# Kernel tuning notes

Measured on AMD Instinct MI355X. Metric: run time of the kernel, lower is better.

The kernel has to match this reference:

```python
import jax, jax.numpy as jnp
import numpy as np

H = 512          # hidden_size
SF = 4           # scale_factor
B, S, L = 16, 2048, 2

def setup_inputs() -> dict:
    key = jax.random.key(0)
    ks = jax.random.split(key, 9)
    return {
        "hidden": jax.random.normal(ks[0], (L, B, H * SF), dtype=jnp.float32),
        "encoder_outputs": jax.random.normal(ks[1], (B, S, H * SF), dtype=jnp.float32),
        "We": jax.random.normal(ks[2], (H, H * SF), dtype=jnp.float32) * 0.02,
        "be": jax.random.normal(ks[3], (H,), dtype=jnp.float32) * 0.02,
        "Wh": jax.random.normal(ks[4], (H, H * SF), dtype=jnp.float32) * 0.02,
        "bh": jax.random.normal(ks[5], (H,), dtype=jnp.float32) * 0.02,
        "Wa": jax.random.normal(ks[6], (H, 2 * H), dtype=jnp.float32) * 0.02,
        "ba": jax.random.normal(ks[7], (H,), dtype=jnp.float32) * 0.02,
        "v": jax.random.uniform(ks[8], (1, H), dtype=jnp.float32),
    }

def reference(hidden, encoder_outputs, We, be, Wh, bh, Wa, ba, v):
    # hidden[-1]: [B, 4H] -> [B, H]
    h = hidden[-1] @ Wh.T + bh
    # encoder_outputs: [B, S, 4H] -> [B, S, H]
    eo = jnp.einsum('bsf,hf->bsh', encoder_outputs, We) + be
    # concat([h broadcast to S, eo]) @ Wa.T == h @ Wa_h.T + eo @ Wa_e.T (split concat matmul)
    Wa_h, Wa_e = Wa[:, :H], Wa[:, H:]
    energy = jnp.tanh(h[:, None, :] @ Wa_h.T + jnp.einsum('bsh,kh->bsk', eo, Wa_e) + ba)  # [B,S,H]
    scores = jnp.einsum('bsh,h->bs', energy, v[0])           # [B,S]
    attn_weights = jax.nn.softmax(scores, axis=1)            # [B,S]
    context_vector = jnp.einsum('bs,bsh->bh', attn_weights, eo)  # [B,H]
    return (context_vector, attn_weights)
```

## Files before the change

### kernel.cpp

```cpp
#include <hip/hip_runtime.h>

#define HH 512
#define FF 2048
#define BB 16
#define SS 2048
#define MM 32768

using f32x4 = __attribute__((ext_vector_type(4))) float;
using s16x8 = __attribute__((ext_vector_type(8))) short;

struct __align__(8)  US4 { unsigned short x, y, z, w; };
struct __align__(16) US8 { unsigned short s[8]; };

__device__ __forceinline__ unsigned short f2bf(float f) {
  unsigned int u = __builtin_bit_cast(unsigned int, f);
  u += 0x7fffu + ((u >> 16) & 1u);
  return (unsigned short)(u >> 16);
}
__device__ __forceinline__ float bf2f(unsigned short u) {
  unsigned int x = ((unsigned int)u) << 16;
  return __builtin_bit_cast(float, x);
}
__device__ __forceinline__ void gload_lds16(const void* g, void* l) {
  __builtin_amdgcn_global_load_lds(
      (const __attribute__((address_space(1))) unsigned int*)g,
      (__attribute__((address_space(3))) unsigned int*)l, 16, 0, 0);
}

__global__ void k_conv_we(const float* __restrict__ W, unsigned short* __restrict__ O) {
  int idx = blockIdx.x * 256 + threadIdx.x;
  f32x4 x = *(const f32x4*)(W + idx * 4);
  US4 p{f2bf(x.x), f2bf(x.y), f2bf(x.z), f2bf(x.w)};
  *(US4*)(O + idx * 4) = p;
}
__global__ void k_conv_wae(const float* __restrict__ Wa, unsigned short* __restrict__ O) {
  int idx = blockIdx.x * 256 + threadIdx.x;
  int k = idx >> 7, h4 = idx & 127;
  f32x4 x = *(const f32x4*)(Wa + k * 1024 + 512 + h4 * 4);
  US4 p{f2bf(x.x), f2bf(x.y), f2bf(x.z), f2bf(x.w)};
  *(US4*)(O + idx * 4) = p;
}

__global__ void k_h(const float* __restrict__ hidden, const float* __restrict__ Wh,
                    const float* __restrict__ bh, float* __restrict__ h_ws) {
  int t = threadIdx.x, lane = t & 63, wid = t >> 6;
  int out = blockIdx.x * 4 + wid;
  int b = out >> 9, j = out & 511;
  const float* hr = hidden + (1) * BB * FF + b * FF;
  const float* wr = Wh + j * FF;
  float a = 0.f;
#pragma unroll
  for (int i = 0; i < 8; ++i) {
    int o = i * 256 + lane * 4;
    f32x4 x = *(const f32x4*)(hr + o);
    f32x4 y = *(const f32x4*)(wr + o);
    a += x.x * y.x + x.y * y.y + x.z * y.z + x.w * y.w;
  }
#pragma unroll
  for (int m = 32; m; m >>= 1) a += __shfl_xor(a, m);
  if (lane == 0) h_ws[out] = a + bh[j];
}

__global__ void k_bb(const float* __restrict__ h_ws, const float* __restrict__ Wa,
                     const float* __restrict__ ba, float* __restrict__ bb_ws) {
  int t = threadIdx.x, lane = t & 63, wid = t >> 6;
  int out = blockIdx.x * 4 + wid;
  int b = out >> 9, k = out & 511;
  const float* hr = h_ws + b * HH;
  const float* wa = Wa + k * 1024;
  float a = 0.f;
#pragma unroll
  for (int i = 0; i < 2; ++i) {
    int o = i * 256 + lane * 4;
    f32x4 x = *(const f32x4*)(hr + o);
    f32x4 y = *(const f32x4*)(wa + o);
    a += x.x * y.x + x.y * y.y + x.z * y.z + x.w * y.w;
  }
#pragma unroll
  for (int m = 32; m; m >>= 1) a += __shfl_xor(a, m);
  if (lane == 0) bb_ws[out] = a + ba[k];
}

__global__ __launch_bounds__(512, 4) void k_gemm1(
    const float* __restrict__ enc, const unsigned short* __restrict__ Web,
    const float* __restrict__ be, unsigned short* __restrict__ eo) {
  __shared__ unsigned short smem[36864];
  unsigned short* As = smem;
  unsigned short* Bs = smem + 4096;
  const int t = threadIdx.x, lane = t & 63, wid = t >> 6;
  const int m0 = blockIdx.x * 64;
  f32x4 acc[4][4] = {};

  f32x4 areg[2];
#pragma unroll
  for (int i = 0; i < 2; ++i) {
    int idx = i * 512 + t, row = idx >> 4, c4 = idx & 15;
    areg[i] = *(const f32x4*)(enc + (size_t)(m0 + row) * FF + c4 * 4);
  }

#pragma unroll 1
  for (int kt = 0; kt < FF; kt += 64) {
#pragma unroll
    for (int i = 0; i < 8; ++i) {
      int idx = i * 512 + t, row = idx >> 3, c = idx & 7;
      int sc = c ^ (row & 7);
      gload_lds16(Web + (size_t)row * FF + kt + sc * 8, Bs + idx * 8);
    }
#pragma unroll
    for (int i = 0; i < 2; ++i) {
      int idx = i * 512 + t, row = idx >> 4, c4 = idx & 15;
      f32x4 x = areg[i];
      US4 p{f2bf(x.x), f2bf(x.y), f2bf(x.z), f2bf(x.w)};
      int byte = row * 128 + ((c4 * 8) ^ ((row & 7) << 4));
      *(US4*)((char*)As + byte) = p;
    }
    {
      int ktn = (kt + 64 < FF) ? kt + 64 : 0;
#pragma unroll
      for (int i = 0; i < 2; ++i) {
        int idx = i * 512 + t, row = idx >> 4, c4 = idx & 15;
        areg[i] = *(const f32x4*)(enc + (size_t)(m0 + row) * FF + ktn + c4 * 4);
      }
    }
    __syncthreads();
#pragma unroll
    for (int ks = 0; ks < 2; ++ks) {
      s16x8 af[4], bfr[4];
#pragma unroll
      for (int mi = 0; mi < 4; ++mi) {
        int row = mi * 16 + (lane & 15);
        int byte = row * 128 + ((ks * 64 + (lane >> 4) * 16) ^ ((row & 7) << 4));
        af[mi] = *(const s16x8*)((const char*)As + byte);
      }
#pragma unroll
      for (int ni = 0; ni < 4; ++ni) {
        int row = wid * 64 + ni * 16 + (lane & 15);
        int byte = row * 128 + ((ks * 64 + (lane >> 4) * 16) ^ ((row & 7) << 4));
        bfr[ni] = *(const s16x8*)((const char*)Bs + byte);
      }
#pragma unroll
      for (int mi = 0; mi < 4; ++mi)
#pragma unroll
        for (int ni = 0; ni < 4; ++ni)
          acc[mi][ni] = __builtin_amdgcn_mfma_f32_16x16x32_bf16(af[mi], bfr[ni], acc[mi][ni], 0, 0, 0);
    }
    __syncthreads();
  }

  unsigned short* Cs = smem;
#pragma unroll
  for (int ni = 0; ni < 4; ++ni) {
    int col = wid * 64 + ni * 16 + (lane & 15);
    float bev = be[col];
#pragma unroll
    for (int mi = 0; mi < 4; ++mi)
#pragma unroll
      for (int j = 0; j < 4; ++j) {
        int row = mi * 16 + (lane >> 4) * 4 + j;
        Cs[row * 512 + col] = f2bf(acc[mi][ni][j] + bev);
      }
  }
  __syncthreads();
#pragma unroll
  for (int i = 0; i < 8; ++i) {
    int idx = i * 512 + t, row = idx >> 6, c = idx & 63;
    *(US8*)(eo + (size_t)(m0 + row) * HH + c * 8) = *(const US8*)(Cs + row * 512 + c * 8);
  }
}

__global__ __launch_bounds__(256, 2) void k_gemm2(
    const unsigned short* __restrict__ eo, const unsigned short* __restrict__ Waeb,
    const float* __restrict__ bbw, const float* __restrict__ vv,
    float* __restrict__ sp) {
  __shared__ unsigned short smem[128 * 64 * 2];
  __shared__ float part[2][128];
  unsigned short* As = smem;
  unsigned short* Bs = smem + 128 * 64;
  const int t = threadIdx.x, lane = t & 63;
  const int wid = t >> 6, wr = wid >> 1, wc = wid & 1;
  const int bid = blockIdx.x;
  const int n0 = (bid & 3) * 128;
  const int m0 = (bid >> 2) * 128;
  const int b = m0 >> 11;
  f32x4 acc[4][4] = {};

#pragma unroll 1
  for (int kt = 0; kt < HH; kt += 64) {
#pragma unroll
    for (int i = 0; i < 4; ++i) {
      int idx = i * 256 + t, row = idx >> 3, c = idx & 7;
      int sc = c ^ (row & 7);
      gload_lds16(eo + (size_t)(m0 + row) * HH + kt + sc * 8, As + idx * 8);
    }
#pragma unroll
    for (int i = 0; i < 4; ++i) {
      int idx = i * 256 + t, row = idx >> 3, c = idx & 7;
      int sc = c ^ (row & 7);
      gload_lds16(Waeb + (size_t)(n0 + row) * HH + kt + sc * 8, Bs + idx * 8);
    }
    __syncthreads();
#pragma unroll
    for (int ks = 0; ks < 2; ++ks) {
      s16x8 af[4], bfr[4];
#pragma unroll
      for (int mi = 0; mi < 4; ++mi) {
        int row = wr * 64 + mi * 16 + (lane & 15);
        int byte = row * 128 + ((ks * 64 + (lane >> 4) * 16) ^ ((row & 7) << 4));
        af[mi] = *(const s16x8*)((const char*)As + byte);
      }
#pragma unroll
      for (int ni = 0; ni < 4; ++ni) {
        int row = wc * 64 + ni * 16 + (lane & 15);
        int byte = row * 128 + ((ks * 64 + (lane >> 4) * 16) ^ ((row & 7) << 4));
        bfr[ni] = *(const s16x8*)((const char*)Bs + byte);
      }
#pragma unroll
      for (int mi = 0; mi < 4; ++mi)
#pragma unroll
        for (int ni = 0; ni < 4; ++ni)
          acc[mi][ni] = __builtin_amdgcn_mfma_f32_16x16x32_bf16(af[mi], bfr[ni], acc[mi][ni], 0, 0, 0);
    }
    __syncthreads();
  }

  float vcol[4], bcol[4];
#pragma unroll
  for (int ni = 0; ni < 4; ++ni) {
    int col = n0 + wc * 64 + ni * 16 + (lane & 15);
    vcol[ni] = vv[col];
    bcol[ni] = bbw[b * HH + col];
  }
  float ps[4][4];
#pragma unroll
  for (int mi = 0; mi < 4; ++mi)
#pragma unroll
    for (int j = 0; j < 4; ++j) {
      float s = 0.f;
#pragma unroll
      for (int ni = 0; ni < 4; ++ni)
        s += tanhf(acc[mi][ni][j] + bcol[ni]) * vcol[ni];
      ps[mi][j] = s;
    }
#pragma unroll
  for (int m = 1; m < 16; m <<= 1)
#pragma unroll
    for (int mi = 0; mi < 4; ++mi)
#pragma unroll
      for (int j = 0; j < 4; ++j) ps[mi][j] += __shfl_xor(ps[mi][j], m);
  if ((lane & 15) == 0) {
#pragma unroll
    for (int mi = 0; mi < 4; ++mi)
#pragma unroll
      for (int j = 0; j < 4; ++j)
        part[wc][wr * 64 + mi * 16 + (lane >> 4) * 4 + j] = ps[mi][j];
  }
  __syncthreads();
  if (t < 128) sp[(bid & 3) * MM + m0 + t] = part[0][t] + part[1][t];
}

__global__ void k_softmax(const float* __restrict__ sp, float* __restrict__ attn) {
  const int b = blockIdx.x, t = threadIdx.x, lane = t & 63, wid = t >> 6;
  __shared__ float red[4];
  float vals[8], lmax = -3.0e38f;
#pragma unroll
  for (int i = 0; i < 8; ++i) {
    int s = t + i * 256;
    float x = sp[b * SS + s] + sp[MM + b * SS + s] + sp[2 * MM + b * SS + s] + sp[3 * MM + b * SS + s];
    vals[i] = x;
    lmax = fmaxf(lmax, x);
  }
#pragma unroll
  for (int m = 32; m; m >>= 1) lmax = fmaxf(lmax, __shfl_xor(lmax, m));
  if (lane == 0) red[wid] = lmax;
  __syncthreads();
  lmax = fmaxf(fmaxf(red[0], red[1]), fmaxf(red[2], red[3]));
  __syncthreads();
  float lsum = 0.f;
#pragma unroll
  for (int i = 0; i < 8; ++i) {
    vals[i] = __expf(vals[i] - lmax);
    lsum += vals[i];
  }
#pragma unroll
  for (int m = 32; m; m >>= 1) lsum += __shfl_xor(lsum, m);
  if (lane == 0) red[wid] = lsum;
  __syncthreads();
  float inv = 1.0f / (red[0] + red[1] + red[2] + red[3]);
#pragma unroll
  for (int i = 0; i < 8; ++i) attn[b * SS + t + i * 256] = vals[i] * inv;
}

__global__ __launch_bounds__(512) void k_ctx1(const unsigned short* __restrict__ eo,
                                              const float* __restrict__ attn,
                                              float* __restrict__ cp) {
  __shared__ float red[8][512];
  const int b = blockIdx.x >> 3, ch = blockIdx.x & 7, t = threadIdx.x;
  const int tg = t & 63, sg = t >> 6;
  const float* aw = attn + b * SS + ch * 256;
  float acc[8] = {};
  for (int s = sg; s < 256; s += 8) {
    float w = aw[s];
    US8 vv = *(const US8*)(eo + (size_t)(b * SS + ch * 256 + s) * HH + tg * 8);
#pragma unroll
    for (int j = 0; j < 8; ++j) acc[j] += w * bf2f(vv.s[j]);
  }
#pragma unroll
  for (int j = 0; j < 8; ++j) red[sg][tg * 8 + j] = acc[j];
  __syncthreads();
  float a = 0.f;
#pragma unroll
  for (int g = 0; g < 8; ++g) a += red[g][t];
  cp[blockIdx.x * HH + t] = a;
}

__global__ void k_ctx2(const float* __restrict__ cp, float* __restrict__ ctx) {
  const int b = blockIdx.x, h = threadIdx.x;
  float a = 0.f;
#pragma unroll
  for (int c = 0; c < 8; ++c) a += cp[(b * 8 + c) * HH + h];
  ctx[b * HH + h] = a;
}

extern "C" void kernel_launch(void* const* d_in, const int* in_sizes, int n_in,
                              void* d_out, int out_size, void* d_ws, size_t ws_size,
                              hipStream_t stream) {
  (void)in_sizes; (void)n_in; (void)out_size; (void)ws_size;
  const float* hidden = (const float*)d_in[0];
  const float* enc    = (const float*)d_in[1];
  const float* We     = (const float*)d_in[2];
  const float* be     = (const float*)d_in[3];
  const float* Wh     = (const float*)d_in[4];
  const float* bh     = (const float*)d_in[5];
  const float* Wa     = (const float*)d_in[6];
  const float* ba     = (const float*)d_in[7];
  const float* v      = (const float*)d_in[8];

  float* out  = (float*)d_out;
  float* ctx  = out;
  float* attn = out + BB * HH;

  char* ws = (char*)d_ws;
  unsigned short* Web  = (unsigned short*)ws;  ws += (size_t)HH * FF * 2;
  unsigned short* Waeb = (unsigned short*)ws;  ws += (size_t)HH * HH * 2;
  float* h_ws  = (float*)ws;                   ws += (size_t)BB * HH * 4;
  float* bb_ws = (float*)ws;                   ws += (size_t)BB * HH * 4;
  unsigned short* eo = (unsigned short*)ws;    ws += (size_t)MM * HH * 2;
  float* sp = (float*)ws;                      ws += (size_t)4 * MM * 4;
  float* cp = (float*)ws;                      ws += (size_t)BB * 8 * HH * 4;

  k_conv_we<<<1024, 256, 0, stream>>>(We, Web);
  k_conv_wae<<<256, 256, 0, stream>>>(Wa, Waeb);
  k_h<<<2048, 256, 0, stream>>>(hidden, Wh, bh, h_ws);
  k_bb<<<2048, 256, 0, stream>>>(h_ws, Wa, ba, bb_ws);
  k_gemm1<<<512, 512, 0, stream>>>(enc, Web, be, eo);
  k_gemm2<<<1024, 256, 0, stream>>>(eo, Waeb, bb_ws, v, sp);
  k_softmax<<<16, 256, 0, stream>>>(sp, attn);
  k_ctx1<<<128, 512, 0, stream>>>(eo, attn, cp);
  k_ctx2<<<16, 512, 0, stream>>>(cp, ctx);
}
```

Before: 179.1 us.

## Fuse energy GEMM into encoder GEMM with double-buffered pipelined main loop

Merges the second GEMM (eo·Wa_e, tanh, v-dot) into the first GEMM's epilogue. The eo tile stays in LDS and full-width score rows are produced per block, which removes the eo re-read and the four-way partial-score buffer. The main K-loop is rewritten with double-buffered LDS, async global-to-LDS loads and explicit waitcnt/barrier scheduling to overlap loads with MFMA. Weight conversions are merged into one launch and the context reduction gets finer chunking. In exchange, LDS use is larger and occupancy lower, and the second-GEMM B operand is read directly from global memory.

New measurement: 187.3 us. 4.6% more time.

```diff
diff --git a/kernel.cpp b/kernel.cpp
--- a/kernel.cpp
+++ b/kernel.cpp
@@ -1,4 +1,5 @@
 #include <hip/hip_runtime.h>
+#include <math.h>
 
 #define HH 512
 #define FF 2048
@@ -27,18 +28,21 @@
       (__attribute__((address_space(3))) unsigned int*)l, 16, 0, 0);
 }
 
-__global__ void k_conv_we(const float* __restrict__ W, unsigned short* __restrict__ O) {
-  int idx = blockIdx.x * 256 + threadIdx.x;
-  f32x4 x = *(const f32x4*)(W + idx * 4);
-  US4 p{f2bf(x.x), f2bf(x.y), f2bf(x.z), f2bf(x.w)};
-  *(US4*)(O + idx * 4) = p;
-}
-__global__ void k_conv_wae(const float* __restrict__ Wa, unsigned short* __restrict__ O) {
-  int idx = blockIdx.x * 256 + threadIdx.x;
-  int k = idx >> 7, h4 = idx & 127;
-  f32x4 x = *(const f32x4*)(Wa + k * 1024 + 512 + h4 * 4);
-  US4 p{f2bf(x.x), f2bf(x.y), f2bf(x.z), f2bf(x.w)};
-  *(US4*)(O + idx * 4) = p;
+__global__ void k_conv(const float* __restrict__ We, const float* __restrict__ Wa,
+                       unsigned short* __restrict__ OWe, unsigned short* __restrict__ OWa) {
+  int bid = blockIdx.x, t = threadIdx.x;
+  if (bid < 1024) {
+    int idx = bid * 256 + t;
+    f32x4 x = *(const f32x4*)(We + (size_t)idx * 4);
+    US4 p{f2bf(x.x), f2bf(x.y), f2bf(x.z), f2bf(x.w)};
+    *(US4*)(OWe + (size_t)idx * 4) = p;
+  } else {
+    int idx = (bid - 1024) * 256 + t;
+    int k = idx >> 7, h4 = idx & 127;
+    f32x4 x = *(const f32x4*)(Wa + (size_t)k * 1024 + 512 + h4 * 4);
+    US4 p{f2bf(x.x), f2bf(x.y), f2bf(x.z), f2bf(x.w)};
+    *(US4*)(OWa + (size_t)idx * 4) = p;
+  }
 }
 
 __global__ void k_h(const float* __restrict__ hidden, const float* __restrict__ Wh,
@@ -47,7 +51,7 @@
   int out = blockIdx.x * 4 + wid;
   int b = out >> 9, j = out & 511;
   const float* hr = hidden + (1) * BB * FF + b * FF;
-  const float* wr = Wh + j * FF;
+  const float* wr = Wh + (size_t)j * FF;
   float a = 0.f;
 #pragma unroll
   for (int i = 0; i < 8; ++i) {
@@ -67,7 +71,7 @@
   int out = blockIdx.x * 4 + wid;
   int b = out >> 9, k = out & 511;
   const float* hr = h_ws + b * HH;
-  const float* wa = Wa + k * 1024;
+  const float* wa = Wa + (size_t)k * 1024;
   float a = 0.f;
 #pragma unroll
   for (int i = 0; i < 2; ++i) {
@@ -81,73 +85,125 @@
   if (lane == 0) bb_ws[out] = a + ba[k];
 }
 
-__global__ __launch_bounds__(512, 4) void k_gemm1(
+
+template<int CUR, bool IB, bool IA, int WN>
+__device__ __forceinline__ void gstep(const float* enc_m0, const unsigned short* Web,
+                                      unsigned short* smem, int kt, int t, int lane, int wid,
+                                      f32x4* regC, f32x4* regN, f32x4 (&acc)[4][4]) {
+  unsigned short* Asc = smem + (CUR ? 4096 : 0);
+  unsigned short* Asn = smem + (CUR ? 0 : 4096);
+  unsigned short* Bsc = smem + (CUR ? 40960 : 8192);
+  unsigned short* Bsn = smem + (CUR ? 8192 : 40960);
+  asm volatile("s_waitcnt vmcnt(%0)" :: "i"(WN) : "memory");
+  __builtin_amdgcn_sched_barrier(0);
+  __builtin_amdgcn_s_barrier();
+  if (IB) {
+#pragma unroll
+    for (int i = 0; i < 8; ++i) {
+      int idx = i * 512 + t, row = idx >> 3, c = idx & 7, sc = c ^ (row & 7);
+      gload_lds16(Web + (size_t)row * FF + (kt + 64) + sc * 8, Bsn + idx * 8);
+    }
+  }
+  __builtin_amdgcn_sched_barrier(0);
+  if (IA) {
+#pragma unroll
+    for (int i = 0; i < 2; ++i) {
+      int idx = i * 512 + t, row = idx >> 4, c4 = idx & 15;
+      regN[i] = *(const f32x4*)(enc_m0 + (size_t)row * FF + (kt + 128) + c4 * 4);
+    }
+  }
+  __builtin_amdgcn_sched_barrier(0);
+#pragma unroll
+  for (int ks = 0; ks < 2; ++ks) {
+    s16x8 af[4], bfr[4];
+#pragma unroll
+    for (int mi = 0; mi < 4; ++mi) {
+      int row = mi * 16 + (lane & 15);
+      int byte = row * 128 + (((ks * 64) + (lane >> 4) * 16) ^ ((row & 7) << 4));
+      af[mi] = *(const s16x8*)((const char*)Asc + byte);
+    }
+#pragma unroll
+    for (int ni = 0; ni < 4; ++ni) {
+      int row = wid * 64 + ni * 16 + (lane & 15);
+      int byte = row * 128 + (((ks * 64) + (lane >> 4) * 16) ^ ((row & 7) << 4));
+      bfr[ni] = *(const s16x8*)((const char*)Bsc + byte);
+    }
+#pragma unroll
+    for (int mi = 0; mi < 4; ++mi)
+#pragma unroll
+      for (int ni = 0; ni < 4; ++ni)
+        acc[mi][ni] = __builtin_amdgcn_mfma_f32_16x16x32_bf16(af[mi], bfr[ni], acc[mi][ni], 0, 0, 0);
+  }
+  if (IB) {
+#pragma unroll
+    for (int i = 0; i < 2; ++i) {
+      int idx = i * 512 + t, row = idx >> 4, c4 = idx & 15;
+      f32x4 x = regC[i];
+      US4 p{f2bf(x.x), f2bf(x.y), f2bf(x.z), f2bf(x.w)};
+      int byte = row * 128 + ((c4 * 8) ^ ((row & 7) << 4));
+      *(US4*)((char*)Asn + byte) = p;
+    }
+  }
+  asm volatile("s_waitcnt lgkmcnt(0)" ::: "memory");
+  __builtin_amdgcn_sched_barrier(0);
+  __builtin_amdgcn_s_barrier();
+}
+
+__global__ __launch_bounds__(512, 2) void k_gemm1f(
     const float* __restrict__ enc, const unsigned short* __restrict__ Web,
-    const float* __restrict__ be, unsigned short* __restrict__ eo) {
-  __shared__ unsigned short smem[36864];
-  unsigned short* As = smem;
-  unsigned short* Bs = smem + 4096;
+    const float* __restrict__ be, const unsigned short* __restrict__ Waeb,
+    const float* __restrict__ bbw, const float* __restrict__ vv,
+    unsigned short* __restrict__ eo, float* __restrict__ sp) {
+  __shared__ unsigned short smem[73728];
   const int t = threadIdx.x, lane = t & 63, wid = t >> 6;
   const int m0 = blockIdx.x * 64;
+  const float* enc_m0 = enc + (size_t)m0 * FF;
+  unsigned short* As0 = smem;
+  unsigned short* Bs0 = smem + 8192;
   f32x4 acc[4][4] = {};
-
-  f32x4 areg[2];
+  f32x4 areg0[2], areg1[2], aP[2];
+
 #pragma unroll
   for (int i = 0; i < 2; ++i) {
     int idx = i * 512 + t, row = idx >> 4, c4 = idx & 15;
-    areg[i] = *(const f32x4*)(enc + (size_t)(m0 + row) * FF + c4 * 4);
-  }
-
+    aP[i] = *(const f32x4*)(enc_m0 + (size_t)row * FF + c4 * 4);
+  }
+  __builtin_amdgcn_sched_barrier(0);
+#pragma unroll
+  for (int i = 0; i < 8; ++i) {
+    int idx = i * 512 + t, row = idx >> 3, c = idx & 7, sc = c ^ (row & 7);
+    gload_lds16(Web + (size_t)row * FF + sc * 8, Bs0 + idx * 8);
+  }
+  __builtin_amdgcn_sched_barrier(0);
+#pragma unroll
+  for (int i = 0; i < 2; ++i) {
+    int idx = i * 512 + t, row = idx >> 4, c4 = idx & 15;
+    areg1[i] = *(const f32x4*)(enc_m0 + (size_t)row * FF + 64 + c4 * 4);
+  }
+  __builtin_amdgcn_sched_barrier(0);
+#pragma unroll
+  for (int i = 0; i < 2; ++i) {
+    int idx = i * 512 + t, row = idx >> 4, c4 = idx & 15;
+    f32x4 x = aP[i];
+    US4 p{f2bf(x.x), f2bf(x.y), f2bf(x.z), f2bf(x.w)};
+    int byte = row * 128 + ((c4 * 8) ^ ((row & 7) << 4));
+    *(US4*)((char*)As0 + byte) = p;
+  }
+  asm volatile("s_waitcnt lgkmcnt(0)" ::: "memory");
+  __builtin_amdgcn_sched_barrier(0);
+  __builtin_amdgcn_s_barrier();
+
+  int kt = 0;
 #pragma unroll 1
-  for (int kt = 0; kt < FF; kt += 64) {
-#pragma unroll
-    for (int i = 0; i < 8; ++i) {
-      int idx = i * 512 + t, row = idx >> 3, c = idx & 7;
-      int sc = c ^ (row & 7);
-      gload_lds16(Web + (size_t)row * FF + kt + sc * 8, Bs + idx * 8);
-    }
-#pragma unroll
-    for (int i = 0; i < 2; ++i) {
-      int idx = i * 512 + t, row = idx >> 4, c4 = idx & 15;
-      f32x4 x = areg[i];
-      US4 p{f2bf(x.x), f2bf(x.y), f2bf(x.z), f2bf(x.w)};
-      int byte = row * 128 + ((c4 * 8) ^ ((row & 7) << 4));
-      *(US4*)((char*)As + byte) = p;
-    }
-    {
-      int ktn = (kt + 64 < FF) ? kt + 64 : 0;
-#pragma unroll
-      for (int i = 0; i < 2; ++i) {
-        int idx = i * 512 + t, row = idx >> 4, c4 = idx & 15;
-        areg[i] = *(const f32x4*)(enc + (size_t)(m0 + row) * FF + ktn + c4 * 4);
-      }
-    }
-    __syncthreads();
-#pragma unroll
-    for (int ks = 0; ks < 2; ++ks) {
-      s16x8 af[4], bfr[4];
-#pragma unroll
-      for (int mi = 0; mi < 4; ++mi) {
-        int row = mi * 16 + (lane & 15);
-        int byte = row * 128 + ((ks * 64 + (lane >> 4) * 16) ^ ((row & 7) << 4));
-        af[mi] = *(const s16x8*)((const char*)As + byte);
-      }
-#pragma unroll
-      for (int ni = 0; ni < 4; ++ni) {
-        int row = wid * 64 + ni * 16 + (lane & 15);
-        int byte = row * 128 + ((ks * 64 + (lane >> 4) * 16) ^ ((row & 7) << 4));
-        bfr[ni] = *(const s16x8*)((const char*)Bs + byte);
-      }
-#pragma unroll
-      for (int mi = 0; mi < 4; ++mi)
-#pragma unroll
-        for (int ni = 0; ni < 4; ++ni)
-          acc[mi][ni] = __builtin_amdgcn_mfma_f32_16x16x32_bf16(af[mi], bfr[ni], acc[mi][ni], 0, 0, 0);
-    }
-    __syncthreads();
-  }
-
-  unsigned short* Cs = smem;
+  for (int tt = 0; tt < 15; ++tt) {
+    gstep<0, true, true, 2>(enc_m0, Web, smem, kt, t, lane, wid, areg1, areg0, acc);
+    gstep<1, true, true, 2>(enc_m0, Web, smem, kt + 64, t, lane, wid, areg0, areg1, acc);
+    kt += 128;
+  }
+  gstep<0, true, false, 2>(enc_m0, Web, smem, 1920, t, lane, wid, areg1, areg0, acc);
+  gstep<1, false, false, 0>(enc_m0, Web, smem, 1984, t, lane, wid, areg0, areg1, acc);
+
+  unsigned short* Cs = smem + 40960;
 #pragma unroll
   for (int ni = 0; ni < 4; ++ni) {
     int col = wid * 64 + ni * 16 + (lane & 15);
@@ -157,76 +213,50 @@
 #pragma unroll
       for (int j = 0; j < 4; ++j) {
         int row = mi * 16 + (lane >> 4) * 4 + j;
-        Cs[row * 512 + col] = f2bf(acc[mi][ni][j] + bev);
+        int byte = row * 1024 + ((col * 2) ^ ((row & 7) << 4));
+        *(unsigned short*)((char*)Cs + byte) = f2bf(acc[mi][ni][j] + bev);
       }
   }
   __syncthreads();
+
 #pragma unroll
   for (int i = 0; i < 8; ++i) {
     int idx = i * 512 + t, row = idx >> 6, c = idx & 63;
-    *(US8*)(eo + (size_t)(m0 + row) * HH + c * 8) = *(const US8*)(Cs + row * 512 + c * 8);
-  }
-}
-
-__global__ __launch_bounds__(256, 2) void k_gemm2(
-    const unsigned short* __restrict__ eo, const unsigned short* __restrict__ Waeb,
-    const float* __restrict__ bbw, const float* __restrict__ vv,
-    float* __restrict__ sp) {
-  __shared__ unsigned short smem[128 * 64 * 2];
-  __shared__ float part[2][128];
-  unsigned short* As = smem;
-  unsigned short* Bs = smem + 128 * 64;
-  const int t = threadIdx.x, lane = t & 63;
-  const int wid = t >> 6, wr = wid >> 1, wc = wid & 1;
-  const int bid = blockIdx.x;
-  const int n0 = (bid & 3) * 128;
-  const int m0 = (bid >> 2) * 128;
+    int byte = row * 1024 + ((c * 16) ^ ((row & 7) << 4));
+    *(US8*)(eo + (size_t)(m0 + row) * HH + c * 8) = *(const US8*)((const char*)Cs + byte);
+  }
+
+  f32x4 acc2[4][4] = {};
+#pragma unroll 1
+  for (int kt2 = 0; kt2 < HH; kt2 += 64) {
+#pragma unroll
+    for (int ks = 0; ks < 2; ++ks) {
+      int k2 = kt2 + ks * 32 + (lane >> 4) * 8;
+      s16x8 af[4], bfr[4];
+#pragma unroll
+      for (int mi = 0; mi < 4; ++mi) {
+        int row = mi * 16 + (lane & 15);
+        int byte = row * 1024 + ((k2 * 2) ^ ((row & 7) << 4));
+        af[mi] = *(const s16x8*)((const char*)Cs + byte);
+      }
+#pragma unroll
+      for (int ni = 0; ni < 4; ++ni) {
+        int nrow = wid * 64 + ni * 16 + (lane & 15);
+        bfr[ni] = *(const s16x8*)(Waeb + (size_t)nrow * HH + k2);
+      }
+#pragma unroll
+      for (int mi = 0; mi < 4; ++mi)
+#pragma unroll
+        for (int ni = 0; ni < 4; ++ni)
+          acc2[mi][ni] = __builtin_amdgcn_mfma_f32_16x16x32_bf16(af[mi], bfr[ni], acc2[mi][ni], 0, 0, 0);
+    }
+  }
+
   const int b = m0 >> 11;
-  f32x4 acc[4][4] = {};
-
-#pragma unroll 1
-  for (int kt = 0; kt < HH; kt += 64) {
-#pragma unroll
-    for (int i = 0; i < 4; ++i) {
-      int idx = i * 256 + t, row = idx >> 3, c = idx & 7;
-      int sc = c ^ (row & 7);
-      gload_lds16(eo + (size_t)(m0 + row) * HH + kt + sc * 8, As + idx * 8);
-    }
-#pragma unroll
-    for (int i = 0; i < 4; ++i) {
-      int idx = i * 256 + t, row = idx >> 3, c = idx & 7;
-      int sc = c ^ (row & 7);
-      gload_lds16(Waeb + (size_t)(n0 + row) * HH + kt + sc * 8, Bs + idx * 8);
-    }
-    __syncthreads();
-#pragma unroll
-    for (int ks = 0; ks < 2; ++ks) {
-      s16x8 af[4], bfr[4];
-#pragma unroll
-      for (int mi = 0; mi < 4; ++mi) {
-        int row = wr * 64 + mi * 16 + (lane & 15);
-        int byte = row * 128 + ((ks * 64 + (lane >> 4) * 16) ^ ((row & 7) << 4));
-        af[mi] = *(const s16x8*)((const char*)As + byte);
-      }
-#pragma unroll
-      for (int ni = 0; ni < 4; ++ni) {
-        int row = wc * 64 + ni * 16 + (lane & 15);
-        int byte = row * 128 + ((ks * 64 + (lane >> 4) * 16) ^ ((row & 7) << 4));
-        bfr[ni] = *(const s16x8*)((const char*)Bs + byte);
-      }
-#pragma unroll
-      for (int mi = 0; mi < 4; ++mi)
-#pragma unroll
-        for (int ni = 0; ni < 4; ++ni)
-          acc[mi][ni] = __builtin_amdgcn_mfma_f32_16x16x32_bf16(af[mi], bfr[ni], acc[mi][ni], 0, 0, 0);
-    }
-    __syncthreads();
-  }
-
   float vcol[4], bcol[4];
 #pragma unroll
   for (int ni = 0; ni < 4; ++ni) {
-    int col = n0 + wc * 64 + ni * 16 + (lane & 15);
+    int col = wid * 64 + ni * 16 + (lane & 15);
     vcol[ni] = vv[col];
     bcol[ni] = bbw[b * HH + col];
   }
@@ -238,7 +268,7 @@
       float s = 0.f;
 #pragma unroll
       for (int ni = 0; ni < 4; ++ni)
-        s += tanhf(acc[mi][ni][j] + bcol[ni]) * vcol[ni];
+        s += tanhf(acc2[mi][ni][j] + bcol[ni]) * vcol[ni];
       ps[mi][j] = s;
     }
 #pragma unroll
@@ -247,15 +277,21 @@
     for (int mi = 0; mi < 4; ++mi)
 #pragma unroll
       for (int j = 0; j < 4; ++j) ps[mi][j] += __shfl_xor(ps[mi][j], m);
+  float* red = (float*)smem;
   if ((lane & 15) == 0) {
 #pragma unroll
     for (int mi = 0; mi < 4; ++mi)
 #pragma unroll
       for (int j = 0; j < 4; ++j)
-        part[wc][wr * 64 + mi * 16 + (lane >> 4) * 4 + j] = ps[mi][j];
-  }
-  __syncthreads();
-  if (t < 128) sp[(bid & 3) * MM + m0 + t] = part[0][t] + part[1][t];
+        red[wid * 64 + mi * 16 + (lane >> 4) * 4 + j] = ps[mi][j];
+  }
+  __syncthreads();
+  if (t < 64) {
+    float s = 0.f;
+#pragma unroll
+    for (int w = 0; w < 8; ++w) s += red[w * 64 + t];
+    sp[m0 + t] = s;
+  }
 }
 
 __global__ void k_softmax(const float* __restrict__ sp, float* __restrict__ attn) {
@@ -264,8 +300,7 @@
   float vals[8], lmax = -3.0e38f;
 #pragma unroll
   for (int i = 0; i < 8; ++i) {
-    int s = t + i * 256;
-    float x = sp[b * SS + s] + sp[MM + b * SS + s] + sp[2 * MM + b * SS + s] + sp[3 * MM + b * SS + s];
+    float x = sp[b * SS + t + i * 256];
     vals[i] = x;
     lmax = fmaxf(lmax, x);
   }
@@ -294,15 +329,17 @@
                                               const float* __restrict__ attn,
                                               float* __restrict__ cp) {
   __shared__ float red[8][512];
-  const int b = blockIdx.x >> 3, ch = blockIdx.x & 7, t = threadIdx.x;
+  const int b = blockIdx.x >> 4, ch = blockIdx.x & 15, t = threadIdx.x;
   const int tg = t & 63, sg = t >> 6;
-  const float* aw = attn + b * SS + ch * 256;
+  const float* aw = attn + b * SS + ch * 128;
   float acc[8] = {};
-  for (int s = sg; s < 256; s += 8) {
+#pragma unroll 4
+  for (int i = 0; i < 16; ++i) {
+    int s = sg + i * 8;
     float w = aw[s];
-    US8 vv = *(const US8*)(eo + (size_t)(b * SS + ch * 256 + s) * HH + tg * 8);
-#pragma unroll
-    for (int j = 0; j < 8; ++j) acc[j] += w * bf2f(vv.s[j]);
+    US8 vv8 = *(const US8*)(eo + (size_t)(b * SS + ch * 128 + s) * HH + tg * 8);
+#pragma unroll
+    for (int j = 0; j < 8; ++j) acc[j] += w * bf2f(vv8.s[j]);
   }
 #pragma unroll
   for (int j = 0; j < 8; ++j) red[sg][tg * 8 + j] = acc[j];
@@ -310,14 +347,14 @@
   float a = 0.f;
 #pragma unroll
   for (int g = 0; g < 8; ++g) a += red[g][t];
-  cp[blockIdx.x * HH + t] = a;
+  cp[(size_t)blockIdx.x * HH + t] = a;
 }
 
 __global__ void k_ctx2(const float* __restrict__ cp, float* __restrict__ ctx) {
   const int b = blockIdx.x, h = threadIdx.x;
   float a = 0.f;
 #pragma unroll
-  for (int c = 0; c < 8; ++c) a += cp[(b * 8 + c) * HH + h];
+  for (int c = 0; c < 16; ++c) a += cp[(size_t)(b * 16 + c) * HH + h];
   ctx[b * HH + h] = a;
 }
 
@@ -345,16 +382,14 @@
   float* h_ws  = (float*)ws;                   ws += (size_t)BB * HH * 4;
   float* bb_ws = (float*)ws;                   ws += (size_t)BB * HH * 4;
   unsigned short* eo = (unsigned short*)ws;    ws += (size_t)MM * HH * 2;
-  float* sp = (float*)ws;                      ws += (size_t)4 * MM * 4;
-  float* cp = (float*)ws;                      ws += (size_t)BB * 8 * HH * 4;
-
-  k_conv_we<<<1024, 256, 0, stream>>>(We, Web);
-  k_conv_wae<<<256, 256, 0, stream>>>(Wa, Waeb);
+  float* sp = (float*)ws;                      ws += (size_t)MM * 4;
+  float* cp = (float*)ws;                      ws += (size_t)BB * 16 * HH * 4;
+
+  k_conv<<<1280, 256, 0, stream>>>(We, Wa, Web, Waeb);
   k_h<<<2048, 256, 0, stream>>>(hidden, Wh, bh, h_ws);
   k_bb<<<2048, 256, 0, stream>>>(h_ws, Wa, ba, bb_ws);
-  k_gemm1<<<512, 512, 0, stream>>>(enc, Web, be, eo);
-  k_gemm2<<<1024, 256, 0, stream>>>(eo, Waeb, bb_ws, v, sp);
+  k_gemm1f<<<512, 512, 0, stream>>>(enc, Web, be, Waeb, bb_ws, v, eo, sp);
   k_softmax<<<16, 256, 0, stream>>>(sp, attn);
-  k_ctx1<<<128, 512, 0, stream>>>(eo, attn, cp);
+  k_ctx1<<<256, 512, 0, stream>>>(eo, attn, cp);
   k_ctx2<<<16, 512, 0, stream>>>(cp, ctx);
 }
```
